# Performance work log

Measured on AMD Instinct MI355X. Metric: run time of the kernel, lower is better.

Reference implementation:

```python
import jax, jax.numpy as jnp
import numpy as np

B, DIM, HEADS = 8, 1024, 8
DH = DIM // HEADS            # 128 = dim_head
MFEAT = 621                  # int(DH * log(DH)) performer features
MAXD = 4                     # max_rel_dist
IMG = 10                     # image side; source hardcodes stride 10 in scatter indices
L = IMG * IMG + 1            # geometry forces L = img_dim**2 + 1


def _geometry():
    m, K = MAXD, 2 * MAXD - 1
    base = np.arange(-m + 1, m)
    dx = np.broadcast_to(np.tile(base, K), (L, K * K))
    dy = np.broadcast_to(np.repeat(base, K), (L, K * K))
    x_off = np.concatenate([np.tile(np.arange(IMG), IMG), [0]])[:, None]
    y_off = np.concatenate([np.repeat(np.arange(IMG), IMG), [IMG]])[:, None]
    x_pos, y_pos = dx + x_off, dy + y_off
    diffs = np.abs(dx) + np.abs(dy)
    valid = (x_pos >= 0) & (x_pos < IMG) & (y_pos >= 0) & (y_pos < IMG) & (diffs < m)
    diffs = np.where(valid, diffs, m)  # invalid taps point at the max-dist encoding
    rel_window = (m - 1) * IMG + (m - 1)
    # scatter positions inside the unfold window (stride 10 hardcoded in source)
    indices = np.tile(np.arange(K), K) + np.repeat(np.arange(K) * 10, K)
    return jnp.asarray(diffs), jnp.asarray(valid), jnp.asarray(indices - rel_window)

DIFFS, VALID, OFFSETS = _geometry()  # [L,K2] int, [L,K2] bool, [K2] int


def softmax_kernel(data, proj, is_query, eps=1e-4):
    dn = data.shape[-1] ** -0.25
    ratio = proj.shape[0] ** -0.5
    dd = jnp.einsum('...id,jd->...ij', data * dn, proj)
    diag = (jnp.sum(data ** 2, -1) * (0.5 * dn * dn))[..., None]
    mx = jnp.max(dd, -1, keepdims=True) if is_query else jnp.max(dd)
    return ratio * (jnp.exp(dd - diag - mx) + eps)


def relative_attention(q, rpe, v):
    # q: [b,h,L,MFEAT] kernel features, rpe: [R,MFEAT], v: [b,h,L,DH]
    mde = rpe[-1]                                   # max-distance encoding
    v_sum = v.sum(-2)                               # [b,h,DH]
    q_dot = jnp.einsum('bhlm,rm->bhlr', q, rpe - mde)
    q_rel = jnp.take_along_axis(q_dot, DIFFS[None, None], axis=-1)  # [b,h,L,K2]
    q_rel = jnp.where(VALID[None, None], q_rel, 0.0)
    # gather v at relative offsets (equivalent to the zero-padded unfold +
    # sparse scatter of q_rel in the source, without the dense 67-wide window)
    pos = jnp.arange(L)[:, None] + OFFSETS[None, :]  # [L,K2]
    inb = (pos >= 0) & (pos < L)
    v_g = v[:, :, jnp.clip(pos, 0, L - 1), :]        # [b,h,L,K2,DH]
    v_g = jnp.where(inb[None, None, :, :, None], v_g, 0.0)
    denom = (rpe[DIFFS] - mde).sum(1) + mde * L      # [L,MFEAT]
    D_inv = 1.0 / jnp.einsum('bhlm,lm->bhl', q, denom)
    q_md = jnp.einsum('bhlm,m->bhl', q, mde)
    out = jnp.einsum('bhl,bhd->bhld', q_md, v_sum) + jnp.einsum('bhlk,bhlkd->bhld', q_rel, v_g)
    return out * D_inv[..., None]


def setup_inputs() -> dict:
    key = jax.random.key(0)
    ks = jax.random.split(key, 9)
    s = DIM ** -0.5
    return {
        'x': jax.random.normal(ks[0], (B, L, DIM), jnp.float32),
        'Wq': jax.random.normal(ks[1], (DIM, DIM), jnp.float32) * s,
        'bq': jnp.zeros((DIM,), jnp.float32),
        'Wv': jax.random.normal(ks[2], (DIM, DIM), jnp.float32) * s,
        'bv': jnp.zeros((DIM,), jnp.float32),
        'rpe': jax.random.normal(ks[3], (MAXD + 1, DH), jnp.float32) * 0.02,
        'proj': jax.random.normal(ks[4], (MFEAT, DH), jnp.float32),
        'Wo': jax.random.normal(ks[5], (DIM, DIM), jnp.float32) * s,
        'bo': jnp.zeros((DIM,), jnp.float32),
    }


def reference(x, Wq, bq, Wv, bv, rpe, proj, Wo, bo):
    b = x.shape[0]
    q = (x @ Wq.T + bq).reshape(b, L, HEADS, DH).transpose(0, 2, 1, 3)
    v = (x @ Wv.T + bv).reshape(b, L, HEADS, DH).transpose(0, 2, 1, 3)
    qf = softmax_kernel(q, proj, is_query=True)
    rf = softmax_kernel(rpe[None, None], proj, is_query=False)[0, 0]
    out = relative_attention(qf, rf, v)          # [b,h,L,DH]
    out = out.transpose(0, 2, 1, 3).reshape(b, L, DIM)
    return out @ Wo.T + bo
```

## Files before the change

### kernel.cpp

```cpp
#include <hip/hip_runtime.h>
#include <math.h>

namespace {

typedef __bf16 bf16_t;
typedef bf16_t bf16x8 __attribute__((ext_vector_type(8)));
typedef bf16_t bf16x4 __attribute__((ext_vector_type(4)));
typedef float f32x4 __attribute__((ext_vector_type(4)));

constexpr int B = 8, L = 101, DIM = 1024, H = 8, DH = 128, MF = 621, MFP = 640;
constexpr int BL = B * L;
constexpr int BLP = 832;
constexpr int BH = B * H;
constexpr int RR = BL * H;

constexpr float DN    = 0.29730177875068026f;
constexpr float DN2   = 0.08838834764831845f;
constexpr float RATIO = 0.04012861672f;
constexpr float EPS   = 1e-4f;

constexpr int NX = BL * DIM / 4;
constexpr int NP = MFP * 32;
constexpr int NR = 64 * DH / 4;
constexpr int NW = DIM * DIM / 4;
constexpr int NZ = 3 * (BLP - BL) * DIM / 4;
constexpr int NV = BH * DH / 4;
constexpr int NTOT = NX + NP + NR + 3 * NW + NZ + NV;

__device__ __forceinline__ f32x4 mfma16(bf16x8 a, bf16x8 b, f32x4 c) {
  return __builtin_amdgcn_mfma_f32_16x16x32_bf16(a, b, c, 0, 0, 0);
}

__device__ __forceinline__ void split2(float f, bf16_t& h, bf16_t& l) {
  h = (bf16_t)f;
  l = (bf16_t)(f - (float)h);
}

__device__ __forceinline__ void gload_lds16(const bf16_t* g, bf16_t* l) {
  __builtin_amdgcn_global_load_lds(
      (const __attribute__((address_space(1))) void*)g,
      (__attribute__((address_space(3))) void*)l, 16, 0, 0);
}

__global__ __launch_bounds__(256) void split_all(const float* __restrict__ x,
                                                 const float* __restrict__ proj,
                                                 const float* __restrict__ rpe,
                                                 const float* __restrict__ Wq,
                                                 const float* __restrict__ Wv,
                                                 const float* __restrict__ Wo,
                                                 bf16_t* __restrict__ xh,
                                                 bf16_t* __restrict__ ph,
                                                 bf16_t* __restrict__ rh, bf16_t* __restrict__ rl,
                                                 bf16_t* __restrict__ Wh,
                                                 bf16_t* __restrict__ Woh,
                                                 bf16_t* __restrict__ qh, bf16_t* __restrict__ ql,
                                                 float* __restrict__ vsum) {
  const int u = blockIdx.x * 256 + threadIdx.x;
  if (u >= NTOT) return;
  auto emit2 = [](const float* s4, float sc, bf16_t* dh, bf16_t* dl, size_t off) {
    float4 f = *(const float4*)s4;
    bf16x4 hv, lv; bf16_t h, l;
    split2(f.x * sc, h, l); hv[0] = h; lv[0] = l;
    split2(f.y * sc, h, l); hv[1] = h; lv[1] = l;
    split2(f.z * sc, h, l); hv[2] = h; lv[2] = l;
    split2(f.w * sc, h, l); hv[3] = h; lv[3] = l;
    *(bf16x4*)(dh + off) = hv;
    *(bf16x4*)(dl + off) = lv;
  };
  auto emit1 = [](const float* s4, float sc, bf16_t* dh, size_t off) {
    float4 f = *(const float4*)s4;
    bf16x4 hv;
    hv[0] = (bf16_t)(f.x * sc); hv[1] = (bf16_t)(f.y * sc);
    hv[2] = (bf16_t)(f.z * sc); hv[3] = (bf16_t)(f.w * sc);
    *(bf16x4*)(dh + off) = hv;
  };
  int t = u;
  if (t < NX) { emit1(x + (size_t)t * 4, 1.f, xh, (size_t)t * 4); return; }
  t -= NX;
  if (t < NP) {
    if ((t >> 5) < MF) emit1(proj + (size_t)t * 4, DN, ph, (size_t)t * 4);
    else { bf16x4 z = {}; *(bf16x4*)(ph + (size_t)t * 4) = z; }
    return;
  }
  t -= NP;
  if (t < NR) {
    if (t < 5 * DH / 4) emit2(rpe + (size_t)t * 4, 1.f, rh, rl, (size_t)t * 4);
    else { bf16x4 z = {}; *(bf16x4*)(rh + (size_t)t * 4) = z; *(bf16x4*)(rl + (size_t)t * 4) = z; }
    return;
  }
  t -= NR;
  if (t < NW) { emit1(Wq + (size_t)t * 4, 1.f, Wh, (size_t)t * 4); return; }
  t -= NW;
  if (t < NW) { emit1(Wv + (size_t)t * 4, 1.f, Wh, (size_t)(t + NW) * 4); return; }
  t -= NW;
  if (t < NW) { emit1(Wo + (size_t)t * 4, 1.f, Woh, (size_t)t * 4); return; }
  t -= NW;
  if (t < NZ) {
    const int buf = t / 6144, o = t % 6144;
    bf16_t* dst = (buf == 0) ? xh : (buf == 1) ? qh : ql;
    bf16x4 z = {};
    *(bf16x4*)(dst + (size_t)BL * DIM + (size_t)o * 4) = z;
    return;
  }
  t -= NZ;
  ((float4*)vsum)[t] = make_float4(0.f, 0.f, 0.f, 0.f);
}

template<int MODE>
__global__ __launch_bounds__(256) void gemm128(const bf16_t* __restrict__ Ah,
                                               const bf16_t* __restrict__ Bh,
                                               const float* __restrict__ bias0,
                                               const float* __restrict__ bias1,
                                               float* __restrict__ Cf,
                                               bf16_t* __restrict__ Ch,
                                               bf16_t* __restrict__ Cl,
                                               float* __restrict__ vsum) {
  constexpr int K = 1024, BK = 128, NK = K / BK;
  __shared__ bf16_t lds[2][2][64 * 128];
  const int tid = threadIdx.x;
  const int w = tid >> 6, lane = tid & 63;
  const int wr = w >> 1, wc = w & 1;
  const int l15 = lane & 15, l4 = lane >> 4;
  const int rowBase = blockIdx.y * 64, colBase = blockIdx.x * 64;
  const int r4 = lane >> 4;
  const int cg = lane & 15;
  const bf16_t* src = (w < 2) ? Ah : Bh;
  const int grow0 = ((w < 2) ? rowBase : colBase) + (w & 1) * 32;
  const int ti = (w < 2) ? 0 : 1;
  const int dst0 = (w & 1) * 32 * 128;
  const bf16_t* pe = src + (size_t)(grow0 + r4) * K + ((cg ^ r4) << 3);
  const bf16_t* po = src + (size_t)(grow0 + r4) * K + ((cg ^ r4 ^ 4) << 3);
  auto STAGE = [&](int bf, int k0) {
#pragma unroll
    for (int j = 0; j < 8; ++j)
      gload_lds16(((j & 1) ? po : pe) + (size_t)(4 * j) * K + k0,
                  &lds[bf][ti][dst0 + j * 512]);
  };
  const int ra0 = wr * 32 + l15, ra1 = ra0 + 16;
  const int rb0 = wc * 32 + l15, rb1 = rb0 + 16;
  auto TADDR = [](int row, int kg) { return row * 128 + (((kg) ^ (row & 7)) << 3); };
  f32x4 acc[2][2] = {};
  STAGE(0, 0);
  __syncthreads();
  int bf = 0;
  for (int ks = 0; ks < NK; ++ks) {
    if (ks + 1 < NK) STAGE(bf ^ 1, (ks + 1) * BK);
#pragma unroll
    for (int subk = 0; subk < 4; ++subk) {
      const int kg = subk * 4 + l4;
      bf16x8 a0 = *(const bf16x8*)&lds[bf][0][TADDR(ra0, kg)];
      bf16x8 a1 = *(const bf16x8*)&lds[bf][0][TADDR(ra1, kg)];
      bf16x8 b0 = *(const bf16x8*)&lds[bf][1][TADDR(rb0, kg)];
      bf16x8 b1 = *(const bf16x8*)&lds[bf][1][TADDR(rb1, kg)];
      acc[0][0] = mfma16(a0, b0, acc[0][0]);
      acc[0][1] = mfma16(a0, b1, acc[0][1]);
      acc[1][0] = mfma16(a1, b0, acc[1][0]);
      acc[1][1] = mfma16(a1, b1, acc[1][1]);
    }
    __syncthreads();
    bf ^= 1;
  }
#pragma unroll
  for (int ni = 0; ni < 2; ++ni) {
    const int col = colBase + wc * 32 + ni * 16 + l15;
#pragma unroll
    for (int mi = 0; mi < 2; ++mi) {
      float vpart = 0.f;
      int curb = -1;
#pragma unroll
      for (int r2 = 0; r2 < 4; ++r2) {
        const int row = rowBase + wr * 32 + mi * 16 + l4 * 4 + r2;
        if (row < BL) {
          if (MODE == 0) {
            Cf[(size_t)row * 1024 + col] = acc[mi][ni][r2] + bias0[col];
          } else {
            if (col < 1024) {
              float val = acc[mi][ni][r2] + bias0[col];
              bf16_t h, lo; split2(val, h, lo);
              Ch[(size_t)row * 1024 + col] = h;
              Cl[(size_t)row * 1024 + col] = lo;
            } else {
              const int vcol = col - 1024;
              const float val = acc[mi][ni][r2] + bias1[vcol];
              Cf[(size_t)row * 1024 + vcol] = val;
              const int b = row / L;
              if (b != curb) {
                if (curb >= 0)
                  atomicAdd(&vsum[(size_t)(curb * 8) * DH + vcol], vpart);
                curb = b; vpart = 0.f;
              }
              vpart += val;
            }
          }
        }
      }
      if (MODE == 1 && curb >= 0)
        atomicAdd(&vsum[(size_t)(curb * 8) * DH + (col - 1024)], vpart);
    }
  }
}

__global__ __launch_bounds__(512) void qf3_kernel(const bf16_t* __restrict__ qh,
                                                  const bf16_t* __restrict__ ql,
                                                  const bf16_t* __restrict__ rh,
                                                  const bf16_t* __restrict__ rl,
                                                  const bf16_t* __restrict__ ph,
                                                  const float* __restrict__ rpe,
                                                  float* __restrict__ fd) {
  const int tid = threadIdx.x;
  __shared__ bf16_t Ahl[2][48 * 128];
  __shared__ bf16_t Bch[2][128 * 128];
  __shared__ float rfs[5][MFP];
  __shared__ float diag[32];
  __shared__ float diag5v[8];
  __shared__ float mxs[8][32];
  __shared__ float mxAll[32];
  __shared__ float mxrf[8];
  __shared__ float sred[8][32][5];
  const int w = tid >> 6, lane = tid & 63;
  const int l15 = lane & 15, l4 = lane >> 4;
  const int r0 = blockIdx.x * 32;
  const int r4 = lane >> 4;
  const int cg = lane & 15;
  if (w < 6) {
    const bf16_t* srcA = (w < 2) ? qh : (w < 4) ? ql : (w == 4) ? rh : rl;
    const int arow0 = (w < 4) ? (r0 + (w & 1) * 16) : 0;
    bf16_t* dstA = &Ahl[(w < 4) ? (w >> 1) : (w - 4)][((w < 4) ? (w & 1) * 16 : 32) * 128];
    const bf16_t* peA = srcA + (size_t)(arow0 + r4) * DH + ((cg ^ r4) << 3);
    const bf16_t* poA = srcA + (size_t)(arow0 + r4) * DH + ((cg ^ r4 ^ 4) << 3);
#pragma unroll
    for (int j = 0; j < 4; ++j)
      gload_lds16(((j & 1) ? poA : peA) + (size_t)(4 * j) * DH, dstA + j * 512);
  }
  const bf16_t* peB = ph + (size_t)(w * 16 + r4) * DH + ((cg ^ r4) << 3);
  const bf16_t* poB = ph + (size_t)(w * 16 + r4) * DH + ((cg ^ r4 ^ 4) << 3);
  auto STAGE_B = [&](int buf, int c) {
    const size_t coff = (size_t)c * 128 * DH;
#pragma unroll
    for (int j = 0; j < 4; ++j)
      gload_lds16(((j & 1) ? poB : peB) + coff + (size_t)(4 * j) * DH,
                  &Bch[buf][(w * 16 + j * 4) * 128]);
  };
  if (tid < 256) {
    const int row = tid >> 3, ch = tid & 7;
    const size_t base = (size_t)(r0 + row) * DH + ch * 16;
    float s = 0.f;
#pragma unroll
    for (int t = 0; t < 2; ++t) {
      bf16x8 vh = *(const bf16x8*)(qh + base + t * 8);
      bf16x8 vl = *(const bf16x8*)(ql + base + t * 8);
#pragma unroll
      for (int e = 0; e < 8; ++e) {
        float f = (float)vh[e] + (float)vl[e];
        s += f * f;
      }
    }
    s += __shfl_xor(s, 1, 64); s += __shfl_xor(s, 2, 64); s += __shfl_xor(s, 4, 64);
    if (ch == 0) diag[row] = (0.5f * DN2) * s;
  }
  if (tid < 40) {
    const int row = tid >> 3, ch = tid & 7;
    float s = 0.f;
#pragma unroll
    for (int e = 0; e < 16; ++e) { float f = rpe[row * DH + ch * 16 + e]; s += f * f; }
    s += __shfl_xor(s, 1, 64); s += __shfl_xor(s, 2, 64); s += __shfl_xor(s, 4, 64);
    if (ch == 0) diag5v[row] = (0.5f * DN2) * s;
  }
  auto TADDR = [](int row, int kg) { return row * 128 + (((kg) ^ (row & 7)) << 3); };
  f32x4 acc[2][5] = {};
  f32x4 accr[5] = {};
  STAGE_B(0, 0);
  __syncthreads();
  int buf = 0;
#pragma unroll
  for (int c = 0; c < 5; ++c) {
    if (c + 1 < 5) STAGE_B(buf ^ 1, c + 1);
#pragma unroll
    for (int ks = 0; ks < 4; ++ks) {
      const int kg = ks * 4 + l4;
      bf16x8 a0h = *(const bf16x8*)&Ahl[0][TADDR(l15, kg)];
      bf16x8 a0l = *(const bf16x8*)&Ahl[1][TADDR(l15, kg)];
      bf16x8 a1h = *(const bf16x8*)&Ahl[0][TADDR(16 + l15, kg)];
      bf16x8 a1l = *(const bf16x8*)&Ahl[1][TADDR(16 + l15, kg)];
      bf16x8 arh = *(const bf16x8*)&Ahl[0][TADDR(32 + l15, kg)];
      bf16x8 arl = *(const bf16x8*)&Ahl[1][TADDR(32 + l15, kg)];
      bf16x8 bb  = *(const bf16x8*)&Bch[buf][TADDR(w * 16 + l15, kg)];
      acc[0][c] = mfma16(a0h, bb, acc[0][c]);
      acc[0][c] = mfma16(a0l, bb, acc[0][c]);
      acc[1][c] = mfma16(a1h, bb, acc[1][c]);
      acc[1][c] = mfma16(a1l, bb, acc[1][c]);
      accr[c]   = mfma16(arh, bb, accr[c]);
      accr[c]   = mfma16(arl, bb, accr[c]);
    }
    __syncthreads();
    buf ^= 1;
  }
  float pm[2][4];
#pragma unroll
  for (int mi = 0; mi < 2; ++mi)
#pragma unroll
    for (int r2 = 0; r2 < 4; ++r2) {
      float m = -3.4e38f;
#pragma unroll
      for (int c = 0; c < 5; ++c) {
        const int col = c * 128 + w * 16 + l15;
        float vv = (col < MF) ? acc[mi][c][r2] : -3.4e38f;
        m = fmaxf(m, vv);
      }
      pm[mi][r2] = m;
    }
#pragma unroll
  for (int mask = 1; mask <= 8; mask <<= 1)
#pragma unroll
    for (int mi = 0; mi < 2; ++mi)
#pragma unroll
      for (int r2 = 0; r2 < 4; ++r2)
        pm[mi][r2] = fmaxf(pm[mi][r2], __shfl_xor(pm[mi][r2], mask, 64));
  if (l15 == 0) {
#pragma unroll
    for (int mi = 0; mi < 2; ++mi)
#pragma unroll
      for (int r2 = 0; r2 < 4; ++r2)
        mxs[w][mi * 16 + l4 * 4 + r2] = pm[mi][r2];
  }
  {
    float m = -3.4e38f;
#pragma unroll
    for (int c = 0; c < 5; ++c) {
      const int col = c * 128 + w * 16 + l15;
#pragma unroll
      for (int r2 = 0; r2 < 4; ++r2) {
        const int row5 = l4 * 4 + r2;
        if (row5 < 5 && col < MF) m = fmaxf(m, accr[c][r2]);
      }
    }
#pragma unroll
    for (int mask = 1; mask <= 32; mask <<= 1) m = fmaxf(m, __shfl_xor(m, mask, 64));
    if (lane == 0) mxrf[w] = m;
  }
  __syncthreads();
  {
    float mxR = mxrf[0];
#pragma unroll
    for (int i = 1; i < 8; ++i) mxR = fmaxf(mxR, mxrf[i]);
#pragma unroll
    for (int c = 0; c < 5; ++c) {
      const int col = c * 128 + w * 16 + l15;
#pragma unroll
      for (int r2 = 0; r2 < 4; ++r2) {
        const int row5 = l4 * 4 + r2;
        if (row5 < 5) {
          float val = (col < MF)
              ? RATIO * (__expf(accr[c][r2] - diag5v[row5] - mxR) + EPS) : 0.f;
          rfs[row5][col] = val;
        }
      }
    }
  }
  if (tid < 32) {
    float m = mxs[0][tid];
#pragma unroll
    for (int i = 1; i < 8; ++i) m = fmaxf(m, mxs[i][tid]);
    mxAll[tid] = m;
  }
  __syncthreads();
  for (int i = tid; i < 4 * MFP; i += 512) rfs[i / MFP][i % MFP] -= rfs[4][i % MFP];
  __syncthreads();
  float s[2][4][5] = {};
#pragma unroll
  for (int mi = 0; mi < 2; ++mi)
#pragma unroll
    for (int r2 = 0; r2 < 4; ++r2) {
      const int row = mi * 16 + l4 * 4 + r2;
      const float sub = diag[row] + mxAll[row];
#pragma unroll
      for (int c = 0; c < 5; ++c) {
        const int col = c * 128 + w * 16 + l15;
        const float qfv = RATIO * (__expf(acc[mi][c][r2] - sub) + EPS);
#pragma unroll
        for (int cc = 0; cc < 5; ++cc) s[mi][r2][cc] += qfv * rfs[cc][col];
      }
    }
#pragma unroll
  for (int mask = 1; mask <= 8; mask <<= 1)
#pragma unroll
    for (int mi = 0; mi < 2; ++mi)
#pragma unroll
      for (int r2 = 0; r2 < 4; ++r2)
#pragma unroll
        for (int cc = 0; cc < 5; ++cc)
          s[mi][r2][cc] += __shfl_xor(s[mi][r2][cc], mask, 64);
  if (l15 == 0) {
#pragma unroll
    for (int mi = 0; mi < 2; ++mi)
#pragma unroll
      for (int r2 = 0; r2 < 4; ++r2)
#pragma unroll
        for (int cc = 0; cc < 5; ++cc)
          sred[w][mi * 16 + l4 * 4 + r2][cc] = s[mi][r2][cc];
  }
  __syncthreads();
  if (tid < 160) {
    const int row = tid / 5, cc = tid % 5;
    float acc5 = sred[0][row][cc];
#pragma unroll
    for (int i = 1; i < 8; ++i) acc5 += sred[i][row][cc];
    fd[(size_t)(r0 + row) * 8 + cc] = acc5;
  }
}

__global__ __launch_bounds__(256) void out_kernel(const float* __restrict__ fd,
                                                  const float* __restrict__ v,
                                                  const float* __restrict__ vsum,
                                                  bf16_t* __restrict__ attnh) {
  const int tid = threadIdx.x;
  const int sub = tid >> 7, d = tid & 127;
  const int bh = blockIdx.y, b = bh >> 3, h = bh & 7;
  const int l = blockIdx.x * 2 + sub;
  if (l >= L) return;
  const size_t r = (size_t)(b * L + l) * H + h;
  const float q0 = fd[r * 8 + 0], q1 = fd[r * 8 + 1], q2 = fd[r * 8 + 2],
              q3 = fd[r * 8 + 3], sM = fd[r * 8 + 4];
  float o = sM * vsum[(size_t)bh * DH + d];
  float c0 = 0, c1 = 0, c2 = 0, c3 = 0;
  const int xo = (l < 100) ? (l % 10) : 0;
  const int yo = (l < 100) ? (l / 10) : 10;
#pragma unroll
  for (int k = 0; k < 49; ++k) {
    const int dx = (k % 7) - 3, dy = (k / 7) - 3;
    const int xp = xo + dx, yp = yo + dy;
    const int df = (dx < 0 ? -dx : dx) + (dy < 0 ? -dy : dy);
    if (xp >= 0 && xp < 10 && yp >= 0 && yp < 10 && df < 4) {
      float qq;
      if (df == 0)      { c0 += 1.f; qq = q0; }
      else if (df == 1) { c1 += 1.f; qq = q1; }
      else if (df == 2) { c2 += 1.f; qq = q2; }
      else              { c3 += 1.f; qq = q3; }
      const int pos = l + dx + 10 * dy;
      o += qq * v[(size_t)(b * L + pos) * DIM + h * DH + d];
    }
  }
  const float D = c0 * q0 + c1 * q1 + c2 * q2 + c3 * q3 + (float)L * sM;
  attnh[(size_t)(b * L + l) * DIM + h * DH + d] = (bf16_t)(o / D);
}

}

extern "C" void kernel_launch(void* const* d_in, const int* in_sizes, int n_in,
                              void* d_out, int out_size, void* d_ws, size_t ws_size,
                              hipStream_t stream) {
  const float* x    = (const float*)d_in[0];
  const float* Wq   = (const float*)d_in[1];
  const float* bq   = (const float*)d_in[2];
  const float* Wv   = (const float*)d_in[3];
  const float* bv   = (const float*)d_in[4];
  const float* rpe  = (const float*)d_in[5];
  const float* proj = (const float*)d_in[6];
  const float* Wo   = (const float*)d_in[7];
  const float* bo   = (const float*)d_in[8];

  char* p = (char*)d_ws;
  auto alloc = [&](size_t bytes) { char* r = p; p += (bytes + 255) & ~255ull; return r; };
  bf16_t* xh  = (bf16_t*)alloc((size_t)BLP * DIM * 2);
  bf16_t* Wh  = (bf16_t*)alloc((size_t)2 * DIM * DIM * 2);
  bf16_t* Woh = (bf16_t*)alloc((size_t)DIM * DIM * 2);
  bf16_t* ph  = (bf16_t*)alloc((size_t)MFP * DH * 2);
  bf16_t* rh  = (bf16_t*)alloc((size_t)64 * DH * 2);
  bf16_t* rl  = (bf16_t*)alloc((size_t)64 * DH * 2);
  bf16_t* qh  = (bf16_t*)alloc((size_t)BLP * DIM * 2);
  bf16_t* ql  = (bf16_t*)alloc((size_t)BLP * DIM * 2);
  float*  v   = (float*)alloc((size_t)BL * DIM * 4);
  float*  fd  = (float*)alloc((size_t)RR * 8 * 4);
  float*  vsm = (float*)alloc((size_t)BH * DH * 4);

  split_all<<<(NTOT + 255) / 256, 256, 0, stream>>>(x, proj, rpe, Wq, Wv, Wo,
                                                    xh, ph, rh, rl,
                                                    Wh, Woh, qh, ql, vsm);
  gemm128<1><<<dim3(32, 13), 256, 0, stream>>>(xh, Wh, bq, bv, v, qh, ql, vsm);
  qf3_kernel<<<202, 512, 0, stream>>>(qh, ql, rh, rl, ph, rpe, fd);
  out_kernel<<<dim3((L + 1) / 2, BH), 256, 0, stream>>>(fd, v, vsm, qh);
  gemm128<0><<<dim3(16, 13), 256, 0, stream>>>(qh, Woh, bo, nullptr,
                                               (float*)d_out, nullptr, nullptr, nullptr);
}
```

Measured before the change: 68.60 us.

## Fuse fp32-to-bf16 conversion into GEMM and feature kernels, drop split_all pass

Removes the standalone split_all kernel that converted x, weights, proj and rpe to bf16 in global memory. The GEMMs now load fp32 tiles into registers, convert them, and write swizzled bf16 into LDS, overlapping the next tile's load with the current MFMA loop. qf3 converts proj and rpe on the fly the same way, and vsum is zeroed with a memset. This saves one kernel launch and a full write-then-read of bf16 copies. In exchange each GEMM block reads twice the bytes in fp32, converts the same weights once per row-block, and uses plain register loads instead of asynchronous global-to-LDS copies, so register pressure rises.

After: 77.99 us. 13.7% more time.

```diff
diff --git a/kernel.cpp b/kernel.cpp
--- a/kernel.cpp
+++ b/kernel.cpp
@@ -5,7 +5,6 @@
 
 typedef __bf16 bf16_t;
 typedef bf16_t bf16x8 __attribute__((ext_vector_type(8)));
-typedef bf16_t bf16x4 __attribute__((ext_vector_type(4)));
 typedef float f32x4 __attribute__((ext_vector_type(4)));
 
 constexpr int B = 8, L = 101, DIM = 1024, H = 8, DH = 128, MF = 621, MFP = 640;
@@ -19,14 +18,6 @@
 constexpr float RATIO = 0.04012861672f;
 constexpr float EPS   = 1e-4f;
 
-constexpr int NX = BL * DIM / 4;
-constexpr int NP = MFP * 32;
-constexpr int NR = 64 * DH / 4;
-constexpr int NW = DIM * DIM / 4;
-constexpr int NZ = 3 * (BLP - BL) * DIM / 4;
-constexpr int NV = BH * DH / 4;
-constexpr int NTOT = NX + NP + NR + 3 * NW + NZ + NV;
-
 __device__ __forceinline__ f32x4 mfma16(bf16x8 a, bf16x8 b, f32x4 c) {
   return __builtin_amdgcn_mfma_f32_16x16x32_bf16(a, b, c, 0, 0, 0);
 }
@@ -34,6 +25,15 @@
 __device__ __forceinline__ void split2(float f, bf16_t& h, bf16_t& l) {
   h = (bf16_t)f;
   l = (bf16_t)(f - (float)h);
+}
+
+__device__ __forceinline__ bf16x8 cvt8(float4 a, float4 b, float sc) {
+  bf16x8 r;
+  r[0] = (bf16_t)(a.x * sc); r[1] = (bf16_t)(a.y * sc);
+  r[2] = (bf16_t)(a.z * sc); r[3] = (bf16_t)(a.w * sc);
+  r[4] = (bf16_t)(b.x * sc); r[5] = (bf16_t)(b.y * sc);
+  r[6] = (bf16_t)(b.z * sc); r[7] = (bf16_t)(b.w * sc);
+  return r;
 }
 
 __device__ __forceinline__ void gload_lds16(const bf16_t* g, bf16_t* l) {
@@ -42,79 +42,17 @@
       (__attribute__((address_space(3))) void*)l, 16, 0, 0);
 }
 
-__global__ __launch_bounds__(256) void split_all(const float* __restrict__ x,
-                                                 const float* __restrict__ proj,
-                                                 const float* __restrict__ rpe,
-                                                 const float* __restrict__ Wq,
-                                                 const float* __restrict__ Wv,
-                                                 const float* __restrict__ Wo,
-                                                 bf16_t* __restrict__ xh,
-                                                 bf16_t* __restrict__ ph,
-                                                 bf16_t* __restrict__ rh, bf16_t* __restrict__ rl,
-                                                 bf16_t* __restrict__ Wh,
-                                                 bf16_t* __restrict__ Woh,
-                                                 bf16_t* __restrict__ qh, bf16_t* __restrict__ ql,
-                                                 float* __restrict__ vsum) {
-  const int u = blockIdx.x * 256 + threadIdx.x;
-  if (u >= NTOT) return;
-  auto emit2 = [](const float* s4, float sc, bf16_t* dh, bf16_t* dl, size_t off) {
-    float4 f = *(const float4*)s4;
-    bf16x4 hv, lv; bf16_t h, l;
-    split2(f.x * sc, h, l); hv[0] = h; lv[0] = l;
-    split2(f.y * sc, h, l); hv[1] = h; lv[1] = l;
-    split2(f.z * sc, h, l); hv[2] = h; lv[2] = l;
-    split2(f.w * sc, h, l); hv[3] = h; lv[3] = l;
-    *(bf16x4*)(dh + off) = hv;
-    *(bf16x4*)(dl + off) = lv;
-  };
-  auto emit1 = [](const float* s4, float sc, bf16_t* dh, size_t off) {
-    float4 f = *(const float4*)s4;
-    bf16x4 hv;
-    hv[0] = (bf16_t)(f.x * sc); hv[1] = (bf16_t)(f.y * sc);
-    hv[2] = (bf16_t)(f.z * sc); hv[3] = (bf16_t)(f.w * sc);
-    *(bf16x4*)(dh + off) = hv;
-  };
-  int t = u;
-  if (t < NX) { emit1(x + (size_t)t * 4, 1.f, xh, (size_t)t * 4); return; }
-  t -= NX;
-  if (t < NP) {
-    if ((t >> 5) < MF) emit1(proj + (size_t)t * 4, DN, ph, (size_t)t * 4);
-    else { bf16x4 z = {}; *(bf16x4*)(ph + (size_t)t * 4) = z; }
-    return;
-  }
-  t -= NP;
-  if (t < NR) {
-    if (t < 5 * DH / 4) emit2(rpe + (size_t)t * 4, 1.f, rh, rl, (size_t)t * 4);
-    else { bf16x4 z = {}; *(bf16x4*)(rh + (size_t)t * 4) = z; *(bf16x4*)(rl + (size_t)t * 4) = z; }
-    return;
-  }
-  t -= NR;
-  if (t < NW) { emit1(Wq + (size_t)t * 4, 1.f, Wh, (size_t)t * 4); return; }
-  t -= NW;
-  if (t < NW) { emit1(Wv + (size_t)t * 4, 1.f, Wh, (size_t)(t + NW) * 4); return; }
-  t -= NW;
-  if (t < NW) { emit1(Wo + (size_t)t * 4, 1.f, Woh, (size_t)t * 4); return; }
-  t -= NW;
-  if (t < NZ) {
-    const int buf = t / 6144, o = t % 6144;
-    bf16_t* dst = (buf == 0) ? xh : (buf == 1) ? qh : ql;
-    bf16x4 z = {};
-    *(bf16x4*)(dst + (size_t)BL * DIM + (size_t)o * 4) = z;
-    return;
-  }
-  t -= NZ;
-  ((float4*)vsum)[t] = make_float4(0.f, 0.f, 0.f, 0.f);
-}
-
 template<int MODE>
-__global__ __launch_bounds__(256) void gemm128(const bf16_t* __restrict__ Ah,
-                                               const bf16_t* __restrict__ Bh,
-                                               const float* __restrict__ bias0,
-                                               const float* __restrict__ bias1,
-                                               float* __restrict__ Cf,
-                                               bf16_t* __restrict__ Ch,
-                                               bf16_t* __restrict__ Cl,
-                                               float* __restrict__ vsum) {
+__global__ __launch_bounds__(256) void gemm128f(const float* __restrict__ Af,
+                                                const bf16_t* __restrict__ Ab,
+                                                const float* __restrict__ B0,
+                                                const float* __restrict__ B1,
+                                                const float* __restrict__ bias0,
+                                                const float* __restrict__ bias1,
+                                                float* __restrict__ Cf,
+                                                bf16_t* __restrict__ Ch,
+                                                bf16_t* __restrict__ Cl,
+                                                float* __restrict__ vsum) {
   constexpr int K = 1024, BK = 128, NK = K / BK;
   __shared__ bf16_t lds[2][2][64 * 128];
   const int tid = threadIdx.x;
@@ -124,27 +62,74 @@
   const int rowBase = blockIdx.y * 64, colBase = blockIdx.x * 64;
   const int r4 = lane >> 4;
   const int cg = lane & 15;
-  const bf16_t* src = (w < 2) ? Ah : Bh;
-  const int grow0 = ((w < 2) ? rowBase : colBase) + (w & 1) * 32;
-  const int ti = (w < 2) ? 0 : 1;
-  const int dst0 = (w & 1) * 32 * 128;
-  const bf16_t* pe = src + (size_t)(grow0 + r4) * K + ((cg ^ r4) << 3);
-  const bf16_t* po = src + (size_t)(grow0 + r4) * K + ((cg ^ r4 ^ 4) << 3);
-  auto STAGE = [&](int bf, int k0) {
+  const bool isA = (w < 2);
+  const int half = w & 1;
+  const int ti = isA ? 0 : 1;
+  const int dst0 = half * 32 * 128;
+  const float* fsrc;
+  int fr0;
+  if (isA) {
+    fsrc = Af;
+    fr0 = rowBase + half * 32;
+  } else {
+    if (MODE == 1) {
+      fsrc = (colBase < 1024) ? B0 : B1;
+      fr0 = ((colBase < 1024) ? colBase : colBase - 1024) + half * 32;
+    } else {
+      fsrc = B0;
+      fr0 = colBase + half * 32;
+    }
+  }
+  const bf16_t* peA = nullptr;
+  const bf16_t* poA = nullptr;
+  if (MODE == 0 && isA) {
+    const int g0 = rowBase + half * 32;
+    peA = Ab + (size_t)(g0 + r4) * K + ((cg ^ r4) << 3);
+    poA = Ab + (size_t)(g0 + r4) * K + ((cg ^ r4 ^ 4) << 3);
+  }
+  float4 va[16];
+  auto LOADREGS = [&](int k0) {
+#pragma unroll
+    for (int j = 0; j < 8; ++j) {
+      int row = fr0 + 4 * j + r4;
+      if (MODE == 1 && isA) row = (row < BL) ? row : (BL - 1);
+      const float* rp = fsrc + (size_t)row * K + k0 + cg * 8;
+      va[2 * j]     = *(const float4*)rp;
+      va[2 * j + 1] = *(const float4*)(rp + 4);
+    }
+  };
+  auto CONVWRITE = [&](int bf) {
+#pragma unroll
+    for (int j = 0; j < 8; ++j) {
+      bf16x8 v8 = cvt8(va[2 * j], va[2 * j + 1], 1.f);
+      const int off = dst0 + (4 * j + r4) * 128 + ((cg ^ ((4 * (j & 1)) | r4)) << 3);
+      *(bf16x8*)&lds[bf][ti][off] = v8;
+    }
+  };
+  auto STAGE_A16 = [&](int bf, int k0) {
 #pragma unroll
     for (int j = 0; j < 8; ++j)
-      gload_lds16(((j & 1) ? po : pe) + (size_t)(4 * j) * K + k0,
-                  &lds[bf][ti][dst0 + j * 512]);
+      gload_lds16(((j & 1) ? poA : peA) + (size_t)(4 * j) * K + k0,
+                  &lds[bf][0][dst0 + j * 512]);
   };
   const int ra0 = wr * 32 + l15, ra1 = ra0 + 16;
   const int rb0 = wc * 32 + l15, rb1 = rb0 + 16;
   auto TADDR = [](int row, int kg) { return row * 128 + (((kg) ^ (row & 7)) << 3); };
   f32x4 acc[2][2] = {};
-  STAGE(0, 0);
+  if (MODE == 0 && isA) {
+    STAGE_A16(0, 0);
+  } else {
+    LOADREGS(0);
+    CONVWRITE(0);
+  }
   __syncthreads();
   int bf = 0;
   for (int ks = 0; ks < NK; ++ks) {
-    if (ks + 1 < NK) STAGE(bf ^ 1, (ks + 1) * BK);
+    const bool more = (ks + 1 < NK);
+    if (more) {
+      if (MODE == 0 && isA) STAGE_A16(bf ^ 1, (ks + 1) * BK);
+      else LOADREGS((ks + 1) * BK);
+    }
 #pragma unroll
     for (int subk = 0; subk < 4; ++subk) {
       const int kg = subk * 4 + l4;
@@ -157,6 +142,7 @@
       acc[1][0] = mfma16(a1, b0, acc[1][0]);
       acc[1][1] = mfma16(a1, b1, acc[1][1]);
     }
+    if (more && !(MODE == 0 && isA)) CONVWRITE(bf ^ 1);
     __syncthreads();
     bf ^= 1;
   }
@@ -202,9 +188,7 @@
 
 __global__ __launch_bounds__(512) void qf3_kernel(const bf16_t* __restrict__ qh,
                                                   const bf16_t* __restrict__ ql,
-                                                  const bf16_t* __restrict__ rh,
-                                                  const bf16_t* __restrict__ rl,
-                                                  const bf16_t* __restrict__ ph,
+                                                  const float* __restrict__ proj,
                                                   const float* __restrict__ rpe,
                                                   float* __restrict__ fd) {
   const int tid = threadIdx.x;
@@ -222,25 +206,62 @@
   const int r0 = blockIdx.x * 32;
   const int r4 = lane >> 4;
   const int cg = lane & 15;
-  if (w < 6) {
-    const bf16_t* srcA = (w < 2) ? qh : (w < 4) ? ql : (w == 4) ? rh : rl;
-    const int arow0 = (w < 4) ? (r0 + (w & 1) * 16) : 0;
-    bf16_t* dstA = &Ahl[(w < 4) ? (w >> 1) : (w - 4)][((w < 4) ? (w & 1) * 16 : 32) * 128];
+  if (w < 4) {
+    const bf16_t* srcA = (w < 2) ? qh : ql;
+    const int arow0 = r0 + (w & 1) * 16;
+    bf16_t* dstA = &Ahl[w >> 1][(w & 1) * 16 * 128];
     const bf16_t* peA = srcA + (size_t)(arow0 + r4) * DH + ((cg ^ r4) << 3);
     const bf16_t* poA = srcA + (size_t)(arow0 + r4) * DH + ((cg ^ r4 ^ 4) << 3);
 #pragma unroll
     for (int j = 0; j < 4; ++j)
       gload_lds16(((j & 1) ? poA : peA) + (size_t)(4 * j) * DH, dstA + j * 512);
-  }
-  const bf16_t* peB = ph + (size_t)(w * 16 + r4) * DH + ((cg ^ r4) << 3);
-  const bf16_t* poB = ph + (size_t)(w * 16 + r4) * DH + ((cg ^ r4 ^ 4) << 3);
-  auto STAGE_B = [&](int buf, int c) {
-    const size_t coff = (size_t)c * 128 * DH;
-#pragma unroll
-    for (int j = 0; j < 4; ++j)
-      gload_lds16(((j & 1) ? poB : peB) + coff + (size_t)(4 * j) * DH,
-                  &Bch[buf][(w * 16 + j * 4) * 128]);
+  } else if (w < 6) {
+#pragma unroll
+    for (int j = 0; j < 2; ++j) {
+      const int row5 = (w - 4) * 8 + 4 * j + r4;
+      bf16x8 h8 = {}, l8 = {};
+      if (row5 < 5) {
+        const float* rp = rpe + (size_t)row5 * DH + cg * 8;
+        float4 p0 = *(const float4*)rp;
+        float4 p1 = *(const float4*)(rp + 4);
+        bf16_t h, l;
+        split2(p0.x, h, l); h8[0] = h; l8[0] = l;
+        split2(p0.y, h, l); h8[1] = h; l8[1] = l;
+        split2(p0.z, h, l); h8[2] = h; l8[2] = l;
+        split2(p0.w, h, l); h8[3] = h; l8[3] = l;
+        split2(p1.x, h, l); h8[4] = h; l8[4] = l;
+        split2(p1.y, h, l); h8[5] = h; l8[5] = l;
+        split2(p1.z, h, l); h8[6] = h; l8[6] = l;
+        split2(p1.w, h, l); h8[7] = h; l8[7] = l;
+      }
+      const int off = (32 + row5) * 128 + ((cg ^ (row5 & 7)) << 3);
+      *(bf16x8*)&Ahl[0][off] = h8;
+      *(bf16x8*)&Ahl[1][off] = l8;
+    }
+  }
+  float4 vb[8];
+  auto LOADB = [&](int c) {
+#pragma unroll
+    for (int j = 0; j < 4; ++j) {
+      int prow = c * 128 + w * 16 + 4 * j + r4;
+      prow = (prow < MF) ? prow : (MF - 1);
+      const float* rp = proj + (size_t)prow * DH + cg * 8;
+      vb[2 * j]     = *(const float4*)rp;
+      vb[2 * j + 1] = *(const float4*)(rp + 4);
+    }
   };
+  auto CONVB = [&](int buf, int c) {
+#pragma unroll
+    for (int j = 0; j < 4; ++j) {
+      const int lrow = w * 16 + 4 * j + r4;
+      const int prow = c * 128 + lrow;
+      bf16x8 v8 = {};
+      if (prow < MF) v8 = cvt8(vb[2 * j], vb[2 * j + 1], DN);
+      const int off = lrow * 128 + ((cg ^ (lrow & 7)) << 3);
+      *(bf16x8*)&Bch[buf][off] = v8;
+    }
+  };
+  LOADB(0);
   if (tid < 256) {
     const int row = tid >> 3, ch = tid & 7;
     const size_t base = (size_t)(r0 + row) * DH + ch * 16;
@@ -266,15 +287,16 @@
     s += __shfl_xor(s, 1, 64); s += __shfl_xor(s, 2, 64); s += __shfl_xor(s, 4, 64);
     if (ch == 0) diag5v[row] = (0.5f * DN2) * s;
   }
+  CONVB(0, 0);
+  __syncthreads();
   auto TADDR = [](int row, int kg) { return row * 128 + (((kg) ^ (row & 7)) << 3); };
   f32x4 acc[2][5] = {};
   f32x4 accr[5] = {};
-  STAGE_B(0, 0);
-  __syncthreads();
   int buf = 0;
 #pragma unroll
   for (int c = 0; c < 5; ++c) {
-    if (c + 1 < 5) STAGE_B(buf ^ 1, c + 1);
+    const bool more = (c + 1 < 5);
+    if (more) LOADB(c + 1);
 #pragma unroll
     for (int ks = 0; ks < 4; ++ks) {
       const int kg = ks * 4 + l4;
@@ -292,6 +314,7 @@
       accr[c]   = mfma16(arh, bb, accr[c]);
       accr[c]   = mfma16(arl, bb, accr[c]);
     }
+    if (more) CONVB(buf ^ 1, c + 1);
     __syncthreads();
     buf ^= 1;
   }
@@ -461,24 +484,17 @@
 
   char* p = (char*)d_ws;
   auto alloc = [&](size_t bytes) { char* r = p; p += (bytes + 255) & ~255ull; return r; };
-  bf16_t* xh  = (bf16_t*)alloc((size_t)BLP * DIM * 2);
-  bf16_t* Wh  = (bf16_t*)alloc((size_t)2 * DIM * DIM * 2);
-  bf16_t* Woh = (bf16_t*)alloc((size_t)DIM * DIM * 2);
-  bf16_t* ph  = (bf16_t*)alloc((size_t)MFP * DH * 2);
-  bf16_t* rh  = (bf16_t*)alloc((size_t)64 * DH * 2);
-  bf16_t* rl  = (bf16_t*)alloc((size_t)64 * DH * 2);
   bf16_t* qh  = (bf16_t*)alloc((size_t)BLP * DIM * 2);
   bf16_t* ql  = (bf16_t*)alloc((size_t)BLP * DIM * 2);
   float*  v   = (float*)alloc((size_t)BL * DIM * 4);
   float*  fd  = (float*)alloc((size_t)RR * 8 * 4);
   float*  vsm = (float*)alloc((size_t)BH * DH * 4);
 
-  split_all<<<(NTOT + 255) / 256, 256, 0, stream>>>(x, proj, rpe, Wq, Wv, Wo,
-                                                    xh, ph, rh, rl,
-                                                    Wh, Woh, qh, ql, vsm);
-  gemm128<1><<<dim3(32, 13), 256, 0, stream>>>(xh, Wh, bq, bv, v, qh, ql, vsm);
-  qf3_kernel<<<202, 512, 0, stream>>>(qh, ql, rh, rl, ph, rpe, fd);
+  hipMemsetAsync(vsm, 0, (size_t)BH * DH * 4, stream);
+  gemm128f<1><<<dim3(32, 13), 256, 0, stream>>>(x, nullptr, Wq, Wv, bq, bv,
+                                                v, qh, ql, vsm);
+  qf3_kernel<<<202, 512, 0, stream>>>(qh, ql, proj, rpe, fd);
   out_kernel<<<dim3((L + 1) / 2, BH), 256, 0, stream>>>(fd, v, vsm, qh);
-  gemm128<0><<<dim3(16, 13), 256, 0, stream>>>(qh, Woh, bo, nullptr,
-                                               (float*)d_out, nullptr, nullptr, nullptr);
-}
+  gemm128f<0><<<dim3(16, 13), 256, 0, stream>>>(nullptr, qh, Wo, nullptr, bo, nullptr,
+                                                (float*)d_out, nullptr, nullptr, nullptr);
+}
```
